# Kernel tuning notes

Hardware: AMD Instinct MI355X
Metric: run time of the kernel (lower is better)

Reference implementation:

```python
import jax, jax.numpy as jnp
import numpy as np

# ---- constants matching the original module's globals ----
H = 16          # self.h: number of bit levels; self.n = h per the source
TP = 8          # self.tp: parallel coordinate channels
N_K = 2         # random masks per flipped bit
T = 512         # T_train: tokens per block
N_TRNBR = 128   # neighbor count
K_VOCAB = 128   # sampled vocab count
N_VOCAB = 50257 # full vocab size V for sampled softmax correction
D = 256         # embedding dim
RATIO_COS = 1.0
RATIO_CRO = 0.1
C_CNC = 2 * H * N_K + 1  # candidate locations per token = 65


def setup_inputs() -> dict:
    key = jax.random.key(0)
    ks = jax.random.split(key, 8)
    n = H  # code: self.n = h
    sta_loc = jax.random.randint(ks[0], (T, TP), 1 - n, n, dtype=jnp.int32)
    nei_loc = jax.random.randint(ks[1], (T, N_TRNBR, TP), 1 - n, n, dtype=jnp.int32)
    voc_loc = jax.random.randint(ks[2], (T, K_VOCAB, TP), 1 - n, n, dtype=jnp.int32)
    sta_emb = jax.random.normal(ks[3], (T, D), dtype=jnp.float32)
    nei_emb = jax.random.normal(ks[4], (T, N_TRNBR, D), dtype=jnp.float32)
    voc_emb = jax.random.normal(ks[5], (T, K_VOCAB, D), dtype=jnp.float32)
    # raw random numbers for generate_random_masks: randint(0, self.n)
    rand_masks = jax.random.randint(ks[6], (T, H, N_K, TP), 0, n, dtype=jnp.int32)
    # converge mode: mask is all ones (generate_mask with converge=True)
    mask = jnp.ones((T, N_TRNBR), dtype=bool)
    return {"sta_loc": sta_loc, "nei_loc": nei_loc, "voc_loc": voc_loc,
            "sta_emb": sta_emb, "nei_emb": nei_emb, "voc_emb": voc_emb,
            "rand_masks": rand_masks, "mask": mask}


def _cos_similarity(c1, c2):
    # sign product: (+1 if >=0 else -1) for each operand
    sg = ((2 * (c1 >= 0).astype(jnp.int32) - 1) *
          (2 * (c2 >= 0).astype(jnp.int32) - 1)).astype(jnp.float32)
    x = ((jnp.abs(c1) ^ jnp.abs(c2)) + 1).astype(jnp.float32)
    # torch.frexp exponent of v>=1 equals floor(log2(v)) + 1
    expo = jnp.floor(jnp.log2(x)) + 1.0
    return sg * (1.0 - expo / H)


def _connection(sta_loc, rand_masks):
    bits = jnp.arange(H, dtype=jnp.int32)
    flip_masks = (1 << bits)                          # [H]
    flipped = sta_loc[:, None, :] ^ flip_masks[None, :, None]  # [T,H,TP]
    # note operator precedence in source: rn & (2**i - 1)
    rm = rand_masks & (flip_masks - 1)[None, :, None, None]    # [T,H,N_K,TP]
    res = (flipped[:, :, None, :] ^ rm).reshape(sta_loc.shape[0], H * N_K, TP)
    return jnp.concatenate([res, sta_loc[:, None, :], -res], axis=1)  # [T,C,TP]


def _normalize(x):
    return x / jnp.maximum(jnp.linalg.norm(x, axis=-1, keepdims=True), 1e-12)


def reference(sta_loc, nei_loc, voc_loc, sta_emb, nei_emb, voc_emb, rand_masks, mask):
    cnc_loc = _connection(sta_loc, rand_masks)          # [T, C, TP]
    lth = mask.sum(axis=1).astype(jnp.float32) + 1e-12  # [T]

    # euclidean-space cosine targets: [T, N_trnbr]
    eu_cos_val = jnp.einsum('td,tnd->tn', _normalize(sta_emb), _normalize(nei_emb))
    # use_eu_norm == True branch: ||sta|| * ||voc|| -> [T, K_vocab]
    eu_cro_nrm = (jnp.linalg.norm(sta_emb, axis=-1, keepdims=True) *
                  jnp.linalg.norm(voc_emb, axis=-1))

    pos_loc = jnp.concatenate([nei_loc, voc_loc], axis=1)           # [T, P, TP]
    cos_sta_pos = _cos_similarity(sta_loc[:, None, :], pos_loc)     # [T, P, TP]
    cos_sta_pos_sum = cos_sta_pos.sum(axis=-1)                      # [T, P]
    cos_cnc_pos = _cos_similarity(cnc_loc[:, None, :, :], pos_loc[:, :, None, :])  # [T,P,C,TP]
    ct_val = (cos_sta_pos_sum[:, :, None, None]
              - cos_sta_pos[:, :, None, :] + cos_cnc_pos) / TP      # [T,P,C,TP]

    # cosine-matching loss over neighbors
    eu = eu_cos_val[:, :, None, None]                               # [T,N,1,1]
    loss_cos = ((ct_val[:, :N_TRNBR] - eu) ** 2 * jnp.abs(eu)
                * mask[:, :, None, None].astype(jnp.float32))
    loss_cos = loss_cos.sum(axis=1) / lth[:, None, None]            # [T, C, TP]

    # sampled softmax CE (uniform proposal), positive class at vocab index 0
    z = ct_val[:, N_TRNBR:] * eu_cro_nrm[:, :, None, None]          # [T, K, C, TP]
    corr = jnp.where(jnp.arange(K_VOCAB) == 0, 0.0,
                     jnp.log(N_VOCAB / K_VOCAB)).astype(jnp.float32)
    zc = z + corr[None, :, None, None]
    loss_cro = jax.scipy.special.logsumexp(zc, axis=1) - zc[:, 0]   # [T, C, TP]

    loss_tot = RATIO_COS * loss_cos + RATIO_CRO * loss_cro

    # get_best_loc with cur_portion=1.0, cur_tp=tp -> pure argmin selection
    idx = jnp.argmin(loss_tot, axis=1)                              # [T, TP]
    gather = lambda a: jnp.take_along_axis(a, idx[:, None, :], axis=1)[:, 0]
    selected_locs = gather(cnc_loc)                                 # [T, TP]
    real_loss_cos = gather(loss_cos).mean(axis=-1)                  # [T]
    real_loss_cro = gather(loss_cro).mean(axis=-1)
    real_loss_tot = gather(loss_tot).mean(axis=-1)
    return selected_locs, real_loss_cos, real_loss_cro, real_loss_tot
```

## Files before the change

### kernel.cpp

```cpp
#include <hip/hip_runtime.h>
#include <math.h>

#define T_DIM 512
#define TP 8
#define NC 65
#define NJ 128
#define LOG2E 1.4426950408889634f
#define LN2   0.6931471805599453f

__device__ __forceinline__ float csim(int va, int vs, int qmix) {
    const int sgn = (vs ^ qmix) & 0x80000000;
    const int x = va ^ (qmix & 0x7fffffff);
    const float u0 = fmaf((float)__clz(x + 1), 0.0625f, -1.0f);
    return __int_as_float(__float_as_int(u0) ^ sgn);
}

__device__ __forceinline__ int make_v(int c, int sta, int rnd_cc_h , int h) {
    const int r = (sta ^ (1 << h)) ^ (rnd_cc_h & ((1 << h) - 1));
    return r;
}

__global__ __launch_bounds__(512, 8) void cg_main(
    const int* __restrict__ sta_loc,
    const int* __restrict__ nei_loc,
    const int* __restrict__ voc_loc,
    const float* __restrict__ sta_emb,
    const float* __restrict__ nei_emb,
    const float* __restrict__ voc_emb,
    const int* __restrict__ rand_masks,
    float* __restrict__ wcos,
    float* __restrict__ wcro)
{
    const int t = blockIdx.x;
    const int side = blockIdx.y;
    const int tid = threadIdx.x;

    __shared__ int2  s_pc[NJ * TP];
    __shared__ float s_w[NJ];
    __shared__ float s_css[NJ];
    __shared__ float s_dot[NJ], s_nn[NJ];
    __shared__ float s_ss;
    __shared__ int   s_sta[TP];
    __shared__ int   s_rand[256];

    if (tid < TP) s_sta[tid] = sta_loc[t * TP + tid];
    if (tid < 256) s_rand[tid] = rand_masks[t * 256 + tid];

    {
        const float* emb = (side == 0) ? nei_emb : voc_emb;
        const int g = tid >> 2, sub = tid & 3;
        const float4* ep = (const float4*)(emb + ((size_t)t * NJ + g) * 256);
        const float4* sp = (const float4*)(sta_emb + (size_t)t * 256);
        float dd = 0.f, nn = 0.f, ss = 0.f;
        #pragma unroll
        for (int i = 0; i < 16; ++i) {
            const int i4 = sub + 4 * i;
            const float4 a = sp[i4];
            const float4 b = ep[i4];
            dd += a.x * b.x + a.y * b.y + a.z * b.z + a.w * b.w;
            nn += b.x * b.x + b.y * b.y + b.z * b.z + b.w * b.w;
            if (g == 0) ss += a.x * a.x + a.y * a.y + a.z * a.z + a.w * a.w;
        }
        dd += __shfl_xor(dd, 1); dd += __shfl_xor(dd, 2);
        nn += __shfl_xor(nn, 1); nn += __shfl_xor(nn, 2);
        if (g == 0) { ss += __shfl_xor(ss, 1); ss += __shfl_xor(ss, 2); }
        if (sub == 0) { s_dot[g] = dd; s_nn[g] = nn; if (g == 0) s_ss = ss; }
    }
    __syncthreads();

    {
        const int* loc = (side == 0) ? nei_loc : voc_loc;
        #pragma unroll
        for (int item = tid; item < NJ * TP; item += 512) {
            const int p = item & 7;
            const int pl = loc[(size_t)t * (NJ * TP) + item];
            const int qm = (pl < 0 ? -pl : pl) | (pl & 0x80000000);
            const int sta = s_sta[p];
            const float csp = csim(sta < 0 ? -sta : sta, sta & 0x80000000, qm);
            s_pc[item].x = qm;
            s_pc[item].y = __float_as_int(csp);
        }
    }
    __syncthreads();

    if (tid < NJ) {
        float cs = 0.f;
        #pragma unroll
        for (int p = 0; p < TP; ++p) cs += __int_as_float(s_pc[tid * TP + p].y);
        s_css[tid] = cs;
        const float ns = sqrtf(s_ss);
        if (side == 0) {
            s_w[tid] = s_dot[tid] / (fmaxf(sqrtf(s_nn[tid]), 1e-12f) * fmaxf(ns, 1e-12f));
        } else {
            s_w[tid] = ns * sqrtf(s_nn[tid]) * (0.125f * LOG2E);
        }
    }
    __syncthreads();

    {
        const float corrl2 = logf(50257.0f / 128.0f) * LOG2E;
        #pragma unroll
        for (int item = tid; item < NJ * TP; item += 512) {
            const int j = item >> 3;
            const float csp = __int_as_float(s_pc[item].y);
            const float b = s_css[j] - csp;
            float val;
            if (side == 0) val = b;
            else val = fmaf(b, s_w[j], (j == 0) ? 0.0f : corrl2);
            s_pc[item].y = __float_as_int(val);
        }
    }
    __syncthreads();

    {
        const int c = tid >> 3, p = tid & 7;
        const int sta = s_sta[p];
        int v;
        if (c == 32) v = sta;
        else {
            const int cc = (c < 32) ? c : (c - 33);
            const int h = cc >> 1;
            const int r = make_v(c, sta, s_rand[cc * TP + p], h);
            v = (c < 32) ? r : -r;
        }
        const int va = v < 0 ? -v : v;
        const int vs = v & 0x80000000;

        if (side == 0) {
            float lc = 0.f;
            #pragma unroll 4
            for (int j = 0; j < NJ; ++j) {
                const int2 pc = s_pc[j * TP + p];
                const float u = csim(va, vs, pc.x);
                const float e = s_w[j];
                const float d = fmaf(__int_as_float(pc.y) + u, 0.125f, -e);
                lc = fmaf(d * d, fabsf(e), lc);
            }
            wcos[((size_t)t * NC + c) * TP + p] = lc * 0.0078125f;
        } else {
            const int2 pc0 = s_pc[p];
            const float u0 = csim(va, vs, pc0.x);
            const float z0 = fmaf(u0, s_w[0], __int_as_float(pc0.y));
            float m = z0, s = 1.0f;
            #pragma unroll 4
            for (int k = 1; k < NJ; ++k) {
                const int2 pc = s_pc[k * TP + p];
                const float u = csim(va, vs, pc.x);
                const float z = fmaf(u, s_w[k], __int_as_float(pc.y));
                const float nm = fmaxf(m, z);
                const float e = exp2f(fminf(z, m) - nm);
                const bool gt = z > m;
                s = fmaf(s, gt ? e : 1.0f, gt ? 1.0f : e);
                m = nm;
            }
            wcro[((size_t)t * NC + c) * TP + p] = (m - z0 + log2f(s)) * LN2;
        }
    }

    {
        const int p = tid >> 6;
        const int lane = tid & 63;
        const int sta = s_sta[p];
        const int v = -((sta ^ (1 << 15)) ^ (s_rand[31 * TP + p] & 0x7fff));
        const int va = v < 0 ? -v : v;
        const int vs = v & 0x80000000;

        if (side == 0) {
            float lc = 0.f;
            #pragma unroll
            for (int jj = 0; jj < 2; ++jj) {
                const int j = 2 * lane + jj;
                const int2 pc = s_pc[j * TP + p];
                const float u = csim(va, vs, pc.x);
                const float e = s_w[j];
                const float d = fmaf(__int_as_float(pc.y) + u, 0.125f, -e);
                lc = fmaf(d * d, fabsf(e), lc);
            }
            #pragma unroll
            for (int off = 1; off < 64; off <<= 1) lc += __shfl_xor(lc, off);
            if (lane == 0) wcos[((size_t)t * NC + 64) * TP + p] = lc * 0.0078125f;
        } else {
            const int ka = 2 * lane, kb = 2 * lane + 1;
            const int2 pa = s_pc[ka * TP + p];
            const int2 pb = s_pc[kb * TP + p];
            const float za = fmaf(csim(va, vs, pa.x), s_w[ka], __int_as_float(pa.y));
            const float zb = fmaf(csim(va, vs, pb.x), s_w[kb], __int_as_float(pb.y));
            float m = fmaxf(za, zb);
            float s = exp2f(za - m) + exp2f(zb - m);
            const float z0 = za;
            #pragma unroll
            for (int off = 1; off < 64; off <<= 1) {
                const float om = __shfl_xor(m, off);
                const float os = __shfl_xor(s, off);
                const float nm = fmaxf(m, om);
                s = fmaf(s, exp2f(m - nm), os * exp2f(om - nm));
                m = nm;
            }
            if (lane == 0) wcro[((size_t)t * NC + 64) * TP + p] = (m - z0 + log2f(s)) * LN2;
        }
    }
}

__global__ __launch_bounds__(64) void cg_fin(
    const int* __restrict__ sta_loc, const int* __restrict__ rand_masks,
    const float* __restrict__ wcos, const float* __restrict__ wcro,
    float* __restrict__ out)
{
    const int t = blockIdx.x;
    const int tid = threadIdx.x;
    float sc = 0.f, sr = 0.f, st = 0.f;
    if (tid < TP) {
        const float* pc = wcos + (size_t)t * NC * TP + tid;
        const float* pr = wcro + (size_t)t * NC * TP + tid;
        float best = INFINITY, blc = 0.f, blr = 0.f;
        int bc = 0;
        for (int c = 0; c < NC; ++c) {
            const float lc = pc[c * TP];
            const float lr = pr[c * TP];
            const float lt = fmaf(0.1f, lr, lc);
            if (lt < best) { best = lt; bc = c; blc = lc; blr = lr; }
        }
        const int sta = sta_loc[t * TP + tid];
        int v;
        if (bc == 32) v = sta;
        else {
            const int cc = (bc < 32) ? bc : (bc - 33);
            const int h = cc >> 1;
            const int r = (sta ^ (1 << h)) ^ (rand_masks[t * 256 + cc * TP + tid] & ((1 << h) - 1));
            v = (bc < 32) ? r : -r;
        }
        out[t * TP + tid] = (float)v;
        sc = blc; sr = blr; st = best;
    }
    sc += __shfl_xor(sc, 1); sc += __shfl_xor(sc, 2); sc += __shfl_xor(sc, 4);
    sr += __shfl_xor(sr, 1); sr += __shfl_xor(sr, 2); sr += __shfl_xor(sr, 4);
    st += __shfl_xor(st, 1); st += __shfl_xor(st, 2); st += __shfl_xor(st, 4);
    if (tid == 0) {
        out[T_DIM * TP + t] = sc * 0.125f;
        out[T_DIM * TP + T_DIM + t] = sr * 0.125f;
        out[T_DIM * TP + 2 * T_DIM + t] = st * 0.125f;
    }
}

extern "C" void kernel_launch(void* const* d_in, const int* in_sizes, int n_in,
                              void* d_out, int out_size, void* d_ws, size_t ws_size,
                              hipStream_t stream) {
    const int* sta_loc = (const int*)d_in[0];
    const int* nei_loc = (const int*)d_in[1];
    const int* voc_loc = (const int*)d_in[2];
    const float* sta_emb = (const float*)d_in[3];
    const float* nei_emb = (const float*)d_in[4];
    const float* voc_emb = (const float*)d_in[5];
    const int* rand_masks = (const int*)d_in[6];
    float* out = (float*)d_out;

    float* wcos = (float*)d_ws;
    float* wcro = wcos + (size_t)T_DIM * NC * TP;

    cg_main<<<dim3(T_DIM, 2), 512, 0, stream>>>(
        sta_loc, nei_loc, voc_loc, sta_emb, nei_emb, voc_emb, rand_masks, wcos, wcro);
    cg_fin<<<T_DIM, 64, 0, stream>>>(sta_loc, rand_masks, wcos, wcro, out);
}
```

Baseline: 218.2 us.

## Use block of 576 threads, precompute per-neighbor terms, and use a global-max softmax

The main kernel now runs with 576 threads so that all 65 candidates times 8 channels get their own thread, replacing the separate wave-reduction path for the last candidate. Per-neighbor constants (offset and weight) are precomputed into an int4 shared-memory layout. The cross-entropy path precomputes a global upper-bound max, so the online-softmax rescaling becomes a plain sum of hardware exp2 values. It also drops the unused dot product for the vocab side, uses a transposed shared array for per-channel sums, and stages the finalize kernel's reads through shared memory. The shared bound max could make the exponentials underflow when it sits far above the actual scores, which is why the sum is clamped before the log.

```diff
diff --git a/kernel.cpp b/kernel.cpp
--- a/kernel.cpp
+++ b/kernel.cpp
@@ -5,22 +5,15 @@
 #define TP 8
 #define NC 65
 #define NJ 128
+#define BLOCK 576
 #define LOG2E 1.4426950408889634f
 #define LN2   0.6931471805599453f
-
-__device__ __forceinline__ float csim(int va, int vs, int qmix) {
-    const int sgn = (vs ^ qmix) & 0x80000000;
-    const int x = va ^ (qmix & 0x7fffffff);
-    const float u0 = fmaf((float)__clz(x + 1), 0.0625f, -1.0f);
-    return __int_as_float(__float_as_int(u0) ^ sgn);
-}
-
-__device__ __forceinline__ int make_v(int c, int sta, int rnd_cc_h , int h) {
-    const int r = (sta ^ (1 << h)) ^ (rnd_cc_h & ((1 << h) - 1));
-    return r;
-}
-
-__global__ __launch_bounds__(512, 8) void cg_main(
+#define CORR_L2 8.617045f
+
+__device__ __forceinline__ float i2f(int x) { return __int_as_float(x); }
+__device__ __forceinline__ int   f2i(float x) { return __float_as_int(x); }
+
+__global__ __launch_bounds__(BLOCK) void cg_main(
     const int* __restrict__ sta_loc,
     const int* __restrict__ nei_loc,
     const int* __restrict__ voc_loc,
@@ -35,10 +28,12 @@
     const int side = blockIdx.y;
     const int tid = threadIdx.x;
 
-    __shared__ int2  s_pc[NJ * TP];
+    __shared__ int4  s_pc4[NJ * TP];
+    __shared__ float s_cspT[TP * 132];
+    __shared__ float s_css[NJ];
     __shared__ float s_w[NJ];
-    __shared__ float s_css[NJ];
     __shared__ float s_dot[NJ], s_nn[NJ];
+    __shared__ float s_Mpart[9 * 8];
     __shared__ float s_ss;
     __shared__ int   s_sta[TP];
     __shared__ int   s_rand[256];
@@ -46,8 +41,8 @@
     if (tid < TP) s_sta[tid] = sta_loc[t * TP + tid];
     if (tid < 256) s_rand[tid] = rand_masks[t * 256 + tid];
 
-    {
-        const float* emb = (side == 0) ? nei_emb : voc_emb;
+    if (tid < 512) {
+        const float* emb = side ? voc_emb : nei_emb;
         const int g = tid >> 2, sub = tid & 3;
         const float4* ep = (const float4*)(emb + ((size_t)t * NJ + g) * 256);
         const float4* sp = (const float4*)(sta_emb + (size_t)t * 256);
@@ -55,30 +50,41 @@
         #pragma unroll
         for (int i = 0; i < 16; ++i) {
             const int i4 = sub + 4 * i;
-            const float4 a = sp[i4];
             const float4 b = ep[i4];
-            dd += a.x * b.x + a.y * b.y + a.z * b.z + a.w * b.w;
             nn += b.x * b.x + b.y * b.y + b.z * b.z + b.w * b.w;
-            if (g == 0) ss += a.x * a.x + a.y * a.y + a.z * a.z + a.w * a.w;
-        }
-        dd += __shfl_xor(dd, 1); dd += __shfl_xor(dd, 2);
+            if (side == 0) {
+                const float4 a = sp[i4];
+                dd += a.x * b.x + a.y * b.y + a.z * b.z + a.w * b.w;
+            }
+            if (g == 0) {
+                const float4 a = sp[i4];
+                ss += a.x * a.x + a.y * a.y + a.z * a.z + a.w * a.w;
+            }
+        }
         nn += __shfl_xor(nn, 1); nn += __shfl_xor(nn, 2);
-        if (g == 0) { ss += __shfl_xor(ss, 1); ss += __shfl_xor(ss, 2); }
-        if (sub == 0) { s_dot[g] = dd; s_nn[g] = nn; if (g == 0) s_ss = ss; }
+        if (side == 0) { dd += __shfl_xor(dd, 1); dd += __shfl_xor(dd, 2); }
+        if (g == 0)    { ss += __shfl_xor(ss, 1); ss += __shfl_xor(ss, 2); }
+        if (sub == 0) {
+            s_nn[g] = nn;
+            if (side == 0) s_dot[g] = dd;
+            if (g == 0) s_ss = ss;
+        }
     }
     __syncthreads();
 
     {
-        const int* loc = (side == 0) ? nei_loc : voc_loc;
-        #pragma unroll
-        for (int item = tid; item < NJ * TP; item += 512) {
-            const int p = item & 7;
-            const int pl = loc[(size_t)t * (NJ * TP) + item];
-            const int qm = (pl < 0 ? -pl : pl) | (pl & 0x80000000);
-            const int sta = s_sta[p];
-            const float csp = csim(sta < 0 ? -sta : sta, sta & 0x80000000, qm);
-            s_pc[item].x = qm;
-            s_pc[item].y = __float_as_int(csp);
+        const int* loc = side ? voc_loc : nei_loc;
+        for (int item = tid; item < NJ * TP; item += BLOCK) {
+            const int pl = loc[t * (NJ * TP) + item];
+            const int qa = pl < 0 ? -pl : pl;
+            const int qsgn = pl & 0x80000000;
+            const int sta = s_sta[item & 7];
+            const int sa = sta < 0 ? -sta : sta;
+            const int x = sa ^ qa;
+            const float u0 = fmaf((float)__clz(x + 1), 0.0625f, -1.0f);
+            const float csp = i2f(f2i(u0) ^ ((sta ^ pl) & 0x80000000));
+            ((int2*)&s_pc4[item])[0] = make_int2(qa, qsgn);
+            s_cspT[(item & 7) * 132 + (item >> 3)] = csp;
         }
     }
     __syncthreads();
@@ -86,33 +92,44 @@
     if (tid < NJ) {
         float cs = 0.f;
         #pragma unroll
-        for (int p = 0; p < TP; ++p) cs += __int_as_float(s_pc[tid * TP + p].y);
+        for (int p = 0; p < TP; ++p) cs += s_cspT[p * 132 + tid];
         s_css[tid] = cs;
         const float ns = sqrtf(s_ss);
-        if (side == 0) {
-            s_w[tid] = s_dot[tid] / (fmaxf(sqrtf(s_nn[tid]), 1e-12f) * fmaxf(ns, 1e-12f));
-        } else {
-            s_w[tid] = ns * sqrtf(s_nn[tid]) * (0.125f * LOG2E);
-        }
+        const float nn = s_nn[tid];
+        if (side == 0)
+            s_w[tid] = s_dot[tid] / (fmaxf(sqrtf(nn), 1e-12f) * fmaxf(ns, 1e-12f));
+        else
+            s_w[tid] = ns * sqrtf(nn) * (0.125f * LOG2E);
     }
     __syncthreads();
 
     {
-        const float corrl2 = logf(50257.0f / 128.0f) * LOG2E;
-        #pragma unroll
-        for (int item = tid; item < NJ * TP; item += 512) {
-            const int j = item >> 3;
-            const float csp = __int_as_float(s_pc[item].y);
+        float mloc = -INFINITY;
+        for (int item = tid; item < NJ * TP; item += BLOCK) {
+            const int j = item >> 3, p = item & 7;
+            const float csp = s_cspT[p * 132 + j];
             const float b = s_css[j] - csp;
-            float val;
-            if (side == 0) val = b;
-            else val = fmaf(b, s_w[j], (j == 0) ? 0.0f : corrl2);
-            s_pc[item].y = __float_as_int(val);
-        }
-    }
-    __syncthreads();
-
-    {
+            const float w = s_w[j];
+            float z2, w2;
+            if (side == 0) { z2 = fmaf(b, 0.125f, -w); w2 = fabsf(w); }
+            else {
+                z2 = fmaf(b, w, j ? CORR_L2 : 0.0f);
+                w2 = w;
+                mloc = fmaxf(mloc, z2 + w);
+            }
+            ((int2*)&s_pc4[item])[1] = make_int2(f2i(z2), f2i(w2));
+        }
+        if (side) {
+            mloc = fmaxf(mloc, __shfl_xor(mloc, 8));
+            mloc = fmaxf(mloc, __shfl_xor(mloc, 16));
+            mloc = fmaxf(mloc, __shfl_xor(mloc, 32));
+            const int lane = tid & 63;
+            if (lane < 8) s_Mpart[(tid >> 6) * 8 + lane] = mloc;
+        }
+    }
+    __syncthreads();
+
+    if (tid < NC * TP) {
         const int c = tid >> 3, p = tid & 7;
         const int sta = s_sta[p];
         int v;
@@ -120,103 +137,95 @@
         else {
             const int cc = (c < 32) ? c : (c - 33);
             const int h = cc >> 1;
-            const int r = make_v(c, sta, s_rand[cc * TP + p], h);
+            const int r = (sta ^ (1 << h)) ^ (s_rand[cc * TP + p] & ((1 << h) - 1));
             v = (c < 32) ? r : -r;
         }
         const int va = v < 0 ? -v : v;
         const int vs = v & 0x80000000;
+        const int4* pc = s_pc4 + p;
 
         if (side == 0) {
-            float lc = 0.f;
-            #pragma unroll 4
-            for (int j = 0; j < NJ; ++j) {
-                const int2 pc = s_pc[j * TP + p];
-                const float u = csim(va, vs, pc.x);
-                const float e = s_w[j];
-                const float d = fmaf(__int_as_float(pc.y) + u, 0.125f, -e);
-                lc = fmaf(d * d, fabsf(e), lc);
-            }
-            wcos[((size_t)t * NC + c) * TP + p] = lc * 0.0078125f;
+            float lc0 = 0.f, lc1 = 0.f;
+            #pragma unroll 2
+            for (int j = 0; j < NJ; j += 2) {
+                const int4 a = pc[j * 8];
+                const int4 b = pc[(j + 1) * 8];
+                {
+                    const int x = va ^ a.x;
+                    const float u8 = fmaf((float)__clz(x + 1), 0.0078125f, -0.125f);
+                    const float d = i2f(f2i(u8) ^ (vs ^ a.y)) + i2f(a.z);
+                    lc0 = fmaf(d * d, i2f(a.w), lc0);
+                }
+                {
+                    const int x = va ^ b.x;
+                    const float u8 = fmaf((float)__clz(x + 1), 0.0078125f, -0.125f);
+                    const float d = i2f(f2i(u8) ^ (vs ^ b.y)) + i2f(b.z);
+                    lc1 = fmaf(d * d, i2f(b.w), lc1);
+                }
+            }
+            wcos[t * (NC * TP) + tid] = (lc0 + lc1) * 0.0078125f;
         } else {
-            const int2 pc0 = s_pc[p];
-            const float u0 = csim(va, vs, pc0.x);
-            const float z0 = fmaf(u0, s_w[0], __int_as_float(pc0.y));
-            float m = z0, s = 1.0f;
-            #pragma unroll 4
-            for (int k = 1; k < NJ; ++k) {
-                const int2 pc = s_pc[k * TP + p];
-                const float u = csim(va, vs, pc.x);
-                const float z = fmaf(u, s_w[k], __int_as_float(pc.y));
-                const float nm = fmaxf(m, z);
-                const float e = exp2f(fminf(z, m) - nm);
-                const bool gt = z > m;
-                s = fmaf(s, gt ? e : 1.0f, gt ? 1.0f : e);
-                m = nm;
-            }
-            wcro[((size_t)t * NC + c) * TP + p] = (m - z0 + log2f(s)) * LN2;
-        }
-    }
-
-    {
-        const int p = tid >> 6;
-        const int lane = tid & 63;
-        const int sta = s_sta[p];
-        const int v = -((sta ^ (1 << 15)) ^ (s_rand[31 * TP + p] & 0x7fff));
-        const int va = v < 0 ? -v : v;
-        const int vs = v & 0x80000000;
-
-        if (side == 0) {
-            float lc = 0.f;
+            float M = s_Mpart[p];
             #pragma unroll
-            for (int jj = 0; jj < 2; ++jj) {
-                const int j = 2 * lane + jj;
-                const int2 pc = s_pc[j * TP + p];
-                const float u = csim(va, vs, pc.x);
-                const float e = s_w[j];
-                const float d = fmaf(__int_as_float(pc.y) + u, 0.125f, -e);
-                lc = fmaf(d * d, fabsf(e), lc);
-            }
-            #pragma unroll
-            for (int off = 1; off < 64; off <<= 1) lc += __shfl_xor(lc, off);
-            if (lane == 0) wcos[((size_t)t * NC + 64) * TP + p] = lc * 0.0078125f;
-        } else {
-            const int ka = 2 * lane, kb = 2 * lane + 1;
-            const int2 pa = s_pc[ka * TP + p];
-            const int2 pb = s_pc[kb * TP + p];
-            const float za = fmaf(csim(va, vs, pa.x), s_w[ka], __int_as_float(pa.y));
-            const float zb = fmaf(csim(va, vs, pb.x), s_w[kb], __int_as_float(pb.y));
-            float m = fmaxf(za, zb);
-            float s = exp2f(za - m) + exp2f(zb - m);
-            const float z0 = za;
-            #pragma unroll
-            for (int off = 1; off < 64; off <<= 1) {
-                const float om = __shfl_xor(m, off);
-                const float os = __shfl_xor(s, off);
-                const float nm = fmaxf(m, om);
-                s = fmaf(s, exp2f(m - nm), os * exp2f(om - nm));
-                m = nm;
-            }
-            if (lane == 0) wcro[((size_t)t * NC + 64) * TP + p] = (m - z0 + log2f(s)) * LN2;
+            for (int w = 1; w < 9; ++w) M = fmaxf(M, s_Mpart[w * 8 + p]);
+            float z0;
+            {
+                const int4 a = pc[0];
+                const int x = va ^ a.x;
+                const float u0 = fmaf((float)__clz(x + 1), 0.0625f, -1.0f);
+                const float u = i2f(f2i(u0) ^ (vs ^ a.y));
+                z0 = fmaf(u, i2f(a.w), i2f(a.z)) - M;
+            }
+            float s0 = __builtin_amdgcn_exp2f(z0), s1;
+            {
+                const int4 a = pc[8];
+                const int x = va ^ a.x;
+                const float u0 = fmaf((float)__clz(x + 1), 0.0625f, -1.0f);
+                const float u = i2f(f2i(u0) ^ (vs ^ a.y));
+                s1 = __builtin_amdgcn_exp2f(fmaf(u, i2f(a.w), i2f(a.z)) - M);
+            }
+            #pragma unroll 2
+            for (int k = 2; k < NJ; k += 2) {
+                const int4 a = pc[k * 8];
+                const int4 b = pc[(k + 1) * 8];
+                {
+                    const int x = va ^ a.x;
+                    const float u0 = fmaf((float)__clz(x + 1), 0.0625f, -1.0f);
+                    const float u = i2f(f2i(u0) ^ (vs ^ a.y));
+                    s0 += __builtin_amdgcn_exp2f(fmaf(u, i2f(a.w), i2f(a.z)) - M);
+                }
+                {
+                    const int x = va ^ b.x;
+                    const float u0 = fmaf((float)__clz(x + 1), 0.0625f, -1.0f);
+                    const float u = i2f(f2i(u0) ^ (vs ^ b.y));
+                    s1 += __builtin_amdgcn_exp2f(fmaf(u, i2f(b.w), i2f(b.z)) - M);
+                }
+            }
+            const float S = fmaxf(s0 + s1, 1e-38f);
+            wcro[t * (NC * TP) + tid] = (__builtin_amdgcn_logf(S) - z0) * LN2;
         }
     }
 }
 
-__global__ __launch_bounds__(64) void cg_fin(
+__global__ __launch_bounds__(128) void cg_fin(
     const int* __restrict__ sta_loc, const int* __restrict__ rand_masks,
     const float* __restrict__ wcos, const float* __restrict__ wcro,
     float* __restrict__ out)
 {
-    const int t = blockIdx.x;
-    const int tid = threadIdx.x;
-    float sc = 0.f, sr = 0.f, st = 0.f;
+    const int t = blockIdx.x, tid = threadIdx.x;
+    __shared__ float sc[NC * TP], sr[NC * TP];
+    for (int i = tid; i < NC * TP; i += 128) {
+        sc[i] = wcos[t * (NC * TP) + i];
+        sr[i] = wcro[t * (NC * TP) + i];
+    }
+    __syncthreads();
+    float vc = 0.f, vr = 0.f, vt = 0.f;
     if (tid < TP) {
-        const float* pc = wcos + (size_t)t * NC * TP + tid;
-        const float* pr = wcro + (size_t)t * NC * TP + tid;
         float best = INFINITY, blc = 0.f, blr = 0.f;
         int bc = 0;
         for (int c = 0; c < NC; ++c) {
-            const float lc = pc[c * TP];
-            const float lr = pr[c * TP];
+            const float lc = sc[c * TP + tid];
+            const float lr = sr[c * TP + tid];
             const float lt = fmaf(0.1f, lr, lc);
             if (lt < best) { best = lt; bc = c; blc = lc; blr = lr; }
         }
@@ -230,15 +239,15 @@
             v = (bc < 32) ? r : -r;
         }
         out[t * TP + tid] = (float)v;
-        sc = blc; sr = blr; st = best;
-    }
-    sc += __shfl_xor(sc, 1); sc += __shfl_xor(sc, 2); sc += __shfl_xor(sc, 4);
-    sr += __shfl_xor(sr, 1); sr += __shfl_xor(sr, 2); sr += __shfl_xor(sr, 4);
-    st += __shfl_xor(st, 1); st += __shfl_xor(st, 2); st += __shfl_xor(st, 4);
+        vc = blc; vr = blr; vt = best;
+    }
+    vc += __shfl_xor(vc, 1); vc += __shfl_xor(vc, 2); vc += __shfl_xor(vc, 4);
+    vr += __shfl_xor(vr, 1); vr += __shfl_xor(vr, 2); vr += __shfl_xor(vr, 4);
+    vt += __shfl_xor(vt, 1); vt += __shfl_xor(vt, 2); vt += __shfl_xor(vt, 4);
     if (tid == 0) {
-        out[T_DIM * TP + t] = sc * 0.125f;
-        out[T_DIM * TP + T_DIM + t] = sr * 0.125f;
-        out[T_DIM * TP + 2 * T_DIM + t] = st * 0.125f;
+        out[T_DIM * TP + t] = vc * 0.125f;
+        out[T_DIM * TP + T_DIM + t] = vr * 0.125f;
+        out[T_DIM * TP + 2 * T_DIM + t] = vt * 0.125f;
     }
 }
 
@@ -257,7 +266,7 @@
     float* wcos = (float*)d_ws;
     float* wcro = wcos + (size_t)T_DIM * NC * TP;
 
-    cg_main<<<dim3(T_DIM, 2), 512, 0, stream>>>(
+    cg_main<<<dim3(T_DIM, 2), BLOCK, 0, stream>>>(
         sta_loc, nei_loc, voc_loc, sta_emb, nei_emb, voc_emb, rand_masks, wcos, wcro);
-    cg_fin<<<T_DIM, 64, 0, stream>>>(sta_loc, rand_masks, wcos, wcro, out);
+    cg_fin<<<T_DIM, 128, 0, stream>>>(sta_loc, rand_masks, wcos, wcro, out);
 }
```

New measurement: 210.1 us. 3.7% less time.
